# Kernel tuning notes

Measured on AMD Instinct MI355X. Metric: run time of the kernel, lower is better.

Reference implementation:

```python
import jax, jax.numpy as jnp
import numpy as np

B, G, D, V = 4, 2048, 256, 60000


def setup_inputs() -> dict:
    key = jax.random.key(0)
    k1, k2, k3, k4, k5 = jax.random.split(key, 5)
    gene_ids = jax.random.randint(k1, (B, G), 0, V, dtype=jnp.int64 if jax.config.jax_enable_x64 else jnp.int32)
    emb_table = jax.random.normal(k2, (V, D), dtype=jnp.float32) * 0.02
    w_proj = jax.random.normal(k3, (2 * D,), dtype=jnp.float32) * (1.0 / np.sqrt(2 * D))
    b_proj = jnp.zeros((), dtype=jnp.float32)
    gate_logits = jax.random.normal(k4, (G * G,), dtype=jnp.float32)
    class_logits = jax.random.normal(k5, (G * G, 3), dtype=jnp.float32)
    return {"gene_ids": gene_ids, "emb_table": emb_table, "w_proj": w_proj,
            "b_proj": b_proj, "gate_logits": gate_logits, "class_logits": class_logits}


def reference(gene_ids, emb_table, w_proj, b_proj, gate_logits, class_logits):
    # Gene embedding lookup: (B, G, D)
    e = emb_table[gene_ids]
    d = e.shape[-1]
    # Linear(2d,1) on cat([e_i, e_j]) == <e_i, w[:d]> + <e_j, w[d:]> + b,
    # broadcast-added over the (i, j) grid — no (B,G,G,2D) concat needed.
    s_i = jnp.einsum("bgd,d->bg", e, w_proj[:d])  # (B, G)
    s_j = jnp.einsum("bgd,d->bg", e, w_proj[d:])  # (B, G)
    interaction = s_i[:, :, None] + s_j[:, None, :] + b_proj  # (B, G, G)

    g = interaction.shape[1]
    # L0 gate, eval mode: hard threshold of sigmoid(gate_logits)
    gate_probs = (jax.nn.sigmoid(gate_logits) > 0.5).astype(e.dtype)  # (G*G,)
    sparse = interaction * gate_probs.reshape(1, g, g)

    # Three-way classifier, eval mode: hard one-hot of argmax(softmax(logits))
    class_probs = jax.nn.one_hot(jnp.argmax(class_logits, axis=-1), 3, dtype=e.dtype)  # (G*G, 3)
    class_values = class_probs @ jnp.array([-1.0, 0.0, 1.0], dtype=e.dtype)  # (G*G,)
    regulatory = sparse * class_values.reshape(1, g, g)

    l0_reg = jnp.sum(jax.nn.sigmoid(gate_logits))
    return (e, interaction, sparse, regulatory, gate_probs, class_probs, l0_reg)
```

## Files before the change

### kernel.cpp

```cpp
#include <hip/hip_runtime.h>

#define BB 4
#define GN 2048
#define DD 256
#define GG (GN * GN)

#define OFF_E   0u
#define OFF_INT 2097152u
#define OFF_SP  18874368u
#define OFF_RG  35651584u
#define OFF_GP  52428800u
#define OFF_CP  56623104u
#define OFF_L0  69206016u

typedef float nat4 __attribute__((ext_vector_type(4)));

__device__ __forceinline__ void nt_store4(float* p, float4 v) {
  nat4 n = {v.x, v.y, v.z, v.w};
  __builtin_nontemporal_store(n, (nat4*)p);
}
__device__ __forceinline__ float4 nt_load4(const float* p) {
  nat4 n = __builtin_nontemporal_load((const nat4*)p);
  return make_float4(n.x, n.y, n.z, n.w);
}

__global__ __launch_bounds__(256) void k_embed(
    const int* __restrict__ gene_ids, const float* __restrict__ emb,
    const float* __restrict__ w, float* __restrict__ e_out,
    float* __restrict__ s_i, float* __restrict__ s_j) {
  const int row  = blockIdx.x * 4 + (threadIdx.x >> 6);
  const int lane = threadIdx.x & 63;
  const int gid  = gene_ids[row];

  const float4 v = ((const float4*)(emb + (size_t)gid * DD))[lane];
  nt_store4(e_out + (size_t)row * DD + lane * 4, v);

  const float4 w0 = ((const float4*)w)[lane];
  const float4 w1 = ((const float4*)(w + DD))[lane];
  float di = v.x * w0.x + v.y * w0.y + v.z * w0.z + v.w * w0.w;
  float dj = v.x * w1.x + v.y * w1.y + v.z * w1.z + v.w * w1.w;
#pragma unroll
  for (int off = 32; off > 0; off >>= 1) {
    di += __shfl_down(di, off);
    dj += __shfl_down(dj, off);
  }
  if (lane == 0) { s_i[row] = di; s_j[row] = dj; }
}

__device__ __forceinline__ int argmax3(float a, float b, float c) {
  int idx = 0; float best = a;
  if (b > best) { best = b; idx = 1; }
  if (c > best) { idx = 2; }
  return idx;
}
__device__ __forceinline__ float sigf(float x) { return 1.0f / (1.0f + __expf(-x)); }

__global__ __launch_bounds__(256) void k_fused(
    const float* __restrict__ gl, const float* __restrict__ cl,
    const float* __restrict__ s_i, const float* __restrict__ s_j,
    const float* __restrict__ bptr,
    float* __restrict__ gate_out, float* __restrict__ cp_out,
    float* __restrict__ inter, float* __restrict__ sparse,
    float* __restrict__ reg, float* __restrict__ l0) {
  const int t  = blockIdx.x * 256 + threadIdx.x;
  const int j4 = t & (GN / 4 - 1);
  const int i  = t >> 9;

  const float4 g  = nt_load4(gl + (size_t)t * 4);
  const float4 c0 = nt_load4(cl + (size_t)t * 12);
  const float4 c1 = nt_load4(cl + (size_t)t * 12 + 4);
  const float4 c2 = nt_load4(cl + (size_t)t * 12 + 8);

  const int i0 = argmax3(c0.x, c0.y, c0.z);
  const int i1 = argmax3(c0.w, c1.x, c1.y);
  const int i2 = argmax3(c1.z, c1.w, c2.x);
  const int i3 = argmax3(c2.y, c2.z, c2.w);

  const float gx = g.x > 0.0f ? 1.0f : 0.0f;
  const float gy = g.y > 0.0f ? 1.0f : 0.0f;
  const float gz = g.z > 0.0f ? 1.0f : 0.0f;
  const float gw = g.w > 0.0f ? 1.0f : 0.0f;

  nt_store4(gate_out + (size_t)t * 4, make_float4(gx, gy, gz, gw));
  nt_store4(cp_out + (size_t)t * 12,
            make_float4(i0 == 0, i0 == 1, i0 == 2, i1 == 0));
  nt_store4(cp_out + (size_t)t * 12 + 4,
            make_float4(i1 == 1, i1 == 2, i2 == 0, i2 == 1));
  nt_store4(cp_out + (size_t)t * 12 + 8,
            make_float4(i2 == 2, i3 == 0, i3 == 1, i3 == 2));

  const float vx = (float)(i0 - 1), vy = (float)(i1 - 1);
  const float vz = (float)(i2 - 1), vw = (float)(i3 - 1);
  const float b0 = bptr[0];

#pragma unroll
  for (int b = 0; b < BB; ++b) {
    const float  si = s_i[b * GN + i] + b0;
    const float4 sj = ((const float4*)(s_j + b * GN))[j4];
    const float4 it4 = make_float4(si + sj.x, si + sj.y, si + sj.z, si + sj.w);
    const float4 sp4 = make_float4(it4.x * gx, it4.y * gy, it4.z * gz, it4.w * gw);
    const float4 rg4 = make_float4(sp4.x * vx, sp4.y * vy, sp4.z * vz, sp4.w * vw);
    const size_t o = (size_t)b * (GG / 4) + t;
    nt_store4(inter  + o * 4, it4);
    nt_store4(sparse + o * 4, sp4);
    nt_store4(reg    + o * 4, rg4);
  }

  float s = sigf(g.x) + sigf(g.y) + sigf(g.z) + sigf(g.w);
#pragma unroll
  for (int off = 32; off > 0; off >>= 1) s += __shfl_down(s, off);
  __shared__ float part[4];
  if ((threadIdx.x & 63) == 0) part[threadIdx.x >> 6] = s;
  __syncthreads();
  if (threadIdx.x == 0) atomicAdd(l0, part[0] + part[1] + part[2] + part[3]);
}

extern "C" void kernel_launch(void* const* d_in, const int* in_sizes, int n_in,
                              void* d_out, int out_size, void* d_ws, size_t ws_size,
                              hipStream_t stream) {
  const int*   gene_ids = (const int*)d_in[0];
  const float* emb      = (const float*)d_in[1];
  const float* w        = (const float*)d_in[2];
  const float* bptr     = (const float*)d_in[3];
  const float* gl       = (const float*)d_in[4];
  const float* cl       = (const float*)d_in[5];
  float* out = (float*)d_out;

  float* s_i = (float*)d_ws;
  float* s_j = s_i + BB * GN;

  (void)hipMemsetAsync(out + OFF_L0, 0, sizeof(float), stream);

  k_embed<<<BB * GN / 4, 256, 0, stream>>>(gene_ids, emb, w, out + OFF_E, s_i, s_j);
  k_fused<<<GG / 1024, 256, 0, stream>>>(gl, cl, s_i, s_j, bptr,
                                         out + OFF_GP, out + OFF_CP,
                                         out + OFF_INT, out + OFF_SP,
                                         out + OFF_RG, out + OFF_L0);
}
```

Before: 397.3 us.

## Stage class logits through LDS for coalesced access, drop nontemporal hints and memset

The fused kernel now loads class_logits and stores class_probs through shared memory, so each wavefront issues contiguous float4 accesses rather than strided 48-byte-per-thread patterns. Nontemporal load and store builtins are replaced with plain vector accesses. The l0 accumulator is zeroed inside the embed kernel, which removes the separate hipMemsetAsync launch. The cost is extra LDS traffic and barriers, and possibly different cache behaviour for the large streaming writes now that the nontemporal hints are gone.

```diff
diff --git a/kernel.cpp b/kernel.cpp
--- a/kernel.cpp
+++ b/kernel.cpp
@@ -13,27 +13,18 @@
 #define OFF_CP  56623104u
 #define OFF_L0  69206016u
 
-typedef float nat4 __attribute__((ext_vector_type(4)));
-
-__device__ __forceinline__ void nt_store4(float* p, float4 v) {
-  nat4 n = {v.x, v.y, v.z, v.w};
-  __builtin_nontemporal_store(n, (nat4*)p);
-}
-__device__ __forceinline__ float4 nt_load4(const float* p) {
-  nat4 n = __builtin_nontemporal_load((const nat4*)p);
-  return make_float4(n.x, n.y, n.z, n.w);
-}
-
 __global__ __launch_bounds__(256) void k_embed(
     const int* __restrict__ gene_ids, const float* __restrict__ emb,
     const float* __restrict__ w, float* __restrict__ e_out,
-    float* __restrict__ s_i, float* __restrict__ s_j) {
+    float* __restrict__ s_i, float* __restrict__ s_j, float* __restrict__ l0) {
+  if (blockIdx.x == 0 && threadIdx.x == 0) *l0 = 0.0f;
+
   const int row  = blockIdx.x * 4 + (threadIdx.x >> 6);
   const int lane = threadIdx.x & 63;
   const int gid  = gene_ids[row];
 
   const float4 v = ((const float4*)(emb + (size_t)gid * DD))[lane];
-  nt_store4(e_out + (size_t)row * DD + lane * 4, v);
+  ((float4*)(e_out + (size_t)row * DD))[lane] = v;
 
   const float4 w0 = ((const float4*)w)[lane];
   const float4 w1 = ((const float4*)(w + DD))[lane];
@@ -62,32 +53,42 @@
     float* __restrict__ gate_out, float* __restrict__ cp_out,
     float* __restrict__ inter, float* __restrict__ sparse,
     float* __restrict__ reg, float* __restrict__ l0) {
-  const int t  = blockIdx.x * 256 + threadIdx.x;
-  const int j4 = t & (GN / 4 - 1);
-  const int i  = t >> 9;
+  __shared__ float4 lds[768];
 
-  const float4 g  = nt_load4(gl + (size_t)t * 4);
-  const float4 c0 = nt_load4(cl + (size_t)t * 12);
-  const float4 c1 = nt_load4(cl + (size_t)t * 12 + 4);
-  const float4 c2 = nt_load4(cl + (size_t)t * 12 + 8);
+  const int tid = threadIdx.x;
+  const int t   = blockIdx.x * 256 + tid;
+  const int j4  = t & (GN / 4 - 1);
+  const int i   = t >> 9;
+  const size_t clBase = (size_t)blockIdx.x * 768;
+
+  const float4* cl4 = (const float4*)cl;
+#pragma unroll
+  for (int k = 0; k < 3; ++k) lds[tid + k * 256] = cl4[clBase + tid + k * 256];
+  __syncthreads();
+  const float4 c0 = lds[tid * 3];
+  const float4 c1 = lds[tid * 3 + 1];
+  const float4 c2 = lds[tid * 3 + 2];
 
   const int i0 = argmax3(c0.x, c0.y, c0.z);
   const int i1 = argmax3(c0.w, c1.x, c1.y);
   const int i2 = argmax3(c1.z, c1.w, c2.x);
   const int i3 = argmax3(c2.y, c2.z, c2.w);
 
+  __syncthreads();
+  lds[tid * 3]     = make_float4(i0 == 0, i0 == 1, i0 == 2, i1 == 0);
+  lds[tid * 3 + 1] = make_float4(i1 == 1, i1 == 2, i2 == 0, i2 == 1);
+  lds[tid * 3 + 2] = make_float4(i2 == 2, i3 == 0, i3 == 1, i3 == 2);
+  __syncthreads();
+  float4* cp4 = (float4*)cp_out;
+#pragma unroll
+  for (int k = 0; k < 3; ++k) cp4[clBase + tid + k * 256] = lds[tid + k * 256];
+
+  const float4 g = ((const float4*)gl)[t];
   const float gx = g.x > 0.0f ? 1.0f : 0.0f;
   const float gy = g.y > 0.0f ? 1.0f : 0.0f;
   const float gz = g.z > 0.0f ? 1.0f : 0.0f;
   const float gw = g.w > 0.0f ? 1.0f : 0.0f;
-
-  nt_store4(gate_out + (size_t)t * 4, make_float4(gx, gy, gz, gw));
-  nt_store4(cp_out + (size_t)t * 12,
-            make_float4(i0 == 0, i0 == 1, i0 == 2, i1 == 0));
-  nt_store4(cp_out + (size_t)t * 12 + 4,
-            make_float4(i1 == 1, i1 == 2, i2 == 0, i2 == 1));
-  nt_store4(cp_out + (size_t)t * 12 + 8,
-            make_float4(i2 == 2, i3 == 0, i3 == 1, i3 == 2));
+  ((float4*)gate_out)[t] = make_float4(gx, gy, gz, gw);
 
   const float vx = (float)(i0 - 1), vy = (float)(i1 - 1);
   const float vz = (float)(i2 - 1), vw = (float)(i3 - 1);
@@ -101,18 +102,18 @@
     const float4 sp4 = make_float4(it4.x * gx, it4.y * gy, it4.z * gz, it4.w * gw);
     const float4 rg4 = make_float4(sp4.x * vx, sp4.y * vy, sp4.z * vz, sp4.w * vw);
     const size_t o = (size_t)b * (GG / 4) + t;
-    nt_store4(inter  + o * 4, it4);
-    nt_store4(sparse + o * 4, sp4);
-    nt_store4(reg    + o * 4, rg4);
+    ((float4*)inter)[o]  = it4;
+    ((float4*)sparse)[o] = sp4;
+    ((float4*)reg)[o]    = rg4;
   }
 
   float s = sigf(g.x) + sigf(g.y) + sigf(g.z) + sigf(g.w);
 #pragma unroll
   for (int off = 32; off > 0; off >>= 1) s += __shfl_down(s, off);
   __shared__ float part[4];
-  if ((threadIdx.x & 63) == 0) part[threadIdx.x >> 6] = s;
+  if ((tid & 63) == 0) part[tid >> 6] = s;
   __syncthreads();
-  if (threadIdx.x == 0) atomicAdd(l0, part[0] + part[1] + part[2] + part[3]);
+  if (tid == 0) atomicAdd(l0, part[0] + part[1] + part[2] + part[3]);
 }
 
 extern "C" void kernel_launch(void* const* d_in, const int* in_sizes, int n_in,
@@ -129,9 +130,8 @@
   float* s_i = (float*)d_ws;
   float* s_j = s_i + BB * GN;
 
-  (void)hipMemsetAsync(out + OFF_L0, 0, sizeof(float), stream);
-
-  k_embed<<<BB * GN / 4, 256, 0, stream>>>(gene_ids, emb, w, out + OFF_E, s_i, s_j);
+  k_embed<<<BB * GN / 4, 256, 0, stream>>>(gene_ids, emb, w, out + OFF_E,
+                                           s_i, s_j, out + OFF_L0);
   k_fused<<<GG / 1024, 256, 0, stream>>>(gl, cl, s_i, s_j, bptr,
                                          out + OFF_GP, out + OFF_CP,
                                          out + OFF_INT, out + OFF_SP,
```

New measurement: 373.8 us. 1.06x faster.
